# Kernel tuning notes

Measured on AMD Instinct MI355X. Metric: run time of the kernel, lower is better.

## Reference

```python
import jax, jax.numpy as jnp
import numpy as np

B, T, I, H = 128, 64, 128, 256
UNFOLDS = 6
EPS = 1e-08


def setup_inputs() -> dict:
    key = jax.random.key(0)
    ks = jax.random.split(key, 12)
    u = lambda k, sh, lo, hi: jax.random.uniform(k, sh, minval=lo, maxval=hi, dtype=jnp.float32)
    return {
        "x": jax.random.normal(ks[0], (B, T, I), dtype=jnp.float32),
        "input_weight": jnp.ones((I,), jnp.float32),
        "input_bias": jnp.zeros((I,), jnp.float32),
        "sensing_mu": u(ks[1], (I, H), 0.3, 0.8),
        "sensing_sigma": u(ks[2], (I, H), 3.0, 8.0),
        "sensing_w": u(ks[3], (I, H), 0.01, 1.0),
        "sensing_erev": 2.0 * jax.random.randint(ks[4], (I, H), 0, 2).astype(jnp.float32) - 1.0,
        "internal_mu": u(ks[5], (H, H), 0.3, 0.8),
        "internal_sigma": u(ks[6], (H, H), 3.0, 8.0),
        "internal_w": u(ks[7], (H, H), 0.01, 1.0),
        "internal_erev": 2.0 * jax.random.randint(ks[8], (H, H), 0, 2).astype(jnp.float32) - 1.0,
        "vleak": u(ks[9], (H,), -0.2, 0.2),
        "gleak": jnp.ones((H,), jnp.float32),
        "cm": jnp.ones((H,), jnp.float32) * 0.5,
        "output_weight": jnp.ones((H,), jnp.float32),
        "output_bias": jnp.zeros((H,), jnp.float32),
    }


def _gate(V, mu, sigma):
    # torch: sigmoid(sigma * (V.unsqueeze(-1) - mu)); V:[B,D] -> [B,D,H]
    return jax.nn.sigmoid(sigma * (V[..., None] - mu))


def reference(x, input_weight, input_bias, sensing_mu, sensing_sigma, sensing_w,
              sensing_erev, internal_mu, internal_sigma, internal_w, internal_erev,
              vleak, gleak, cm, output_weight, output_bias):
    # time_elapsed = 1.0 default -> cm_t = cm / (1/UNFOLDS) = cm * UNFOLDS
    cm_t = cm * UNFOLDS
    gl_vl = gleak * vleak

    def step(V, xt):
        # affine input mapping
        xm = xt * input_weight + input_bias                      # [B, I]
        s_act = sensing_w * _gate(xm, sensing_mu, sensing_sigma)  # [B, I, H]
        w_num_s = jnp.einsum('bih,ih->bh', s_act, sensing_erev)   # sum over I
        w_den_s = s_act.sum(axis=1)                               # [B, H]

        def unfold(Vc, _):
            w_act = internal_w * _gate(Vc, internal_mu, internal_sigma)  # [B, H, H]
            w_num = jnp.einsum('bij,ij->bj', w_act, internal_erev) + w_num_s
            w_den = w_act.sum(axis=1) + w_den_s
            Vn = (Vc * cm_t + gl_vl + w_num) / (cm_t + gleak + w_den + EPS)
            return Vn, None

        V, _ = jax.lax.scan(unfold, V, None, length=UNFOLDS)
        out_t = V * output_weight + output_bias
        return V, out_t

    h0 = jnp.zeros((x.shape[0], cm.shape[0]), x.dtype)
    hT, out = jax.lax.scan(step, h0, jnp.swapaxes(x, 0, 1))  # scan over T
    return jnp.swapaxes(out, 0, 1), hT  # ([B, T, H], [B, H])
```

## Files before the change

### kernel.cpp

```cpp
#include <hip/hip_runtime.h>
#include <hip/hip_fp16.h>

#define B_ 128
#define T_ 64
#define I_ 128
#define H_ 256
#define UF 6
#define EPSF 1e-8f

typedef _Float16 f16x2 __attribute__((ext_vector_type(2)));
union H2U { __half2 h; f16x2 v; unsigned u; };

static __device__ __forceinline__ float rcpf(float x) { return __builtin_amdgcn_rcpf(x); }
static __device__ __forceinline__ unsigned f2h(float f) { return (unsigned)__half_as_ushort(__float2half_rn(f)); }

#define GATE2(VW, AK, BK, WK, NM, DN) {                        \
    H2U v2_; v2_.u = (VW);                                     \
    H2U av_; av_.u = (AK);                                     \
    H2U bv_; bv_.u = (BK);                                     \
    __half2 z_ = __hfma2(av_.h, v2_.h, bv_.h);                 \
    __half2 e_ = h2exp2(z_);                                   \
    __half2 s_ = __hadd2(e_, __float2half2_rn(1.0f));          \
    H2U rv_; rv_.h = h2rcp(s_);                                \
    H2U ws_; ws_.u = (WK);                                     \
    H2U wa_; wa_.u = ws_.u & 0x7fff7fffu;                      \
    NM = __builtin_amdgcn_fdot2(ws_.v, rv_.v, NM, false);      \
    DN = __builtin_amdgcn_fdot2(wa_.v, rv_.v, DN, false);      \
}

__global__ __launch_bounds__(256) void pack_params(
    const float* __restrict__ smu, const float* __restrict__ ssig,
    const float* __restrict__ sw,  const float* __restrict__ serev,
    const float* __restrict__ imu, const float* __restrict__ isig,
    const float* __restrict__ iw,  const float* __restrict__ ierev,
    uint2* __restrict__ ABg, unsigned* __restrict__ Wg,
    uint2* __restrict__ SABg, unsigned* __restrict__ SWg,
    unsigned* __restrict__ Vg4)
{
    const float K = 1.4426950408889634f;
    int idx = blockIdx.x * 256 + threadIdx.x;
    {
        int jh = idx >> 14, rest = idx & 16383;
        int P = rest >> 7, jcol = rest & 127;
        int j = jcol ^ (((P >> 3) & 7) << 1);
        int jg = (jh << 7) + j;
        int i0 = 2 * P, i1 = i0 + 1;
        unsigned a0 = f2h(-isig[i0 * H_ + jg] * K);
        unsigned a1 = f2h(-isig[i1 * H_ + jg] * K);
        unsigned b0 = f2h(isig[i0 * H_ + jg] * imu[i0 * H_ + jg] * K);
        unsigned b1 = f2h(isig[i1 * H_ + jg] * imu[i1 * H_ + jg] * K);
        ABg[idx] = make_uint2(a0 | (a1 << 16), b0 | (b1 << 16));
    }
    {
        int P = idx >> 8, jg = idx & 255;
        int i0 = 2 * P, i1 = i0 + 1;
        unsigned w0 = f2h(iw[i0 * H_ + jg] * ierev[i0 * H_ + jg]);
        unsigned w1 = f2h(iw[i1 * H_ + jg] * ierev[i1 * H_ + jg]);
        Wg[idx] = w0 | (w1 << 16);
    }
    if (idx < 64 * H_) {
        int p = idx >> 8, jg = idx & 255;
        int i0 = 2 * p, i1 = i0 + 1;
        unsigned a0 = f2h(-ssig[i0 * H_ + jg] * K);
        unsigned a1 = f2h(-ssig[i1 * H_ + jg] * K);
        unsigned b0 = f2h(ssig[i0 * H_ + jg] * smu[i0 * H_ + jg] * K);
        unsigned b1 = f2h(ssig[i1 * H_ + jg] * smu[i1 * H_ + jg] * K);
        SABg[idx] = make_uint2(a0 | (a1 << 16), b0 | (b1 << 16));
        unsigned w0 = f2h(sw[i0 * H_ + jg] * serev[i0 * H_ + jg]);
        unsigned w1 = f2h(sw[i1 * H_ + jg] * serev[i1 * H_ + jg]);
        SWg[idx] = w0 | (w1 << 16);
    }
    Vg4[idx] = 0u;
    Vg4[idx + 32768] = 0u;
}

__global__ __launch_bounds__(1024)
__attribute__((amdgpu_waves_per_eu(4, 4)))
void ltc_rec(
    const float* __restrict__ x, const float* __restrict__ in_w, const float* __restrict__ in_b,
    const uint2* __restrict__ ABg, const unsigned* __restrict__ Wg,
    const uint2* __restrict__ SABg, const unsigned* __restrict__ SWg,
    const float* __restrict__ vleak, const float* __restrict__ gleak, const float* __restrict__ cm,
    const float* __restrict__ out_w, const float* __restrict__ out_b,
    unsigned* __restrict__ Vg4,
    float* __restrict__ out, float* __restrict__ hT)
{
    __shared__ __align__(16) unsigned char L[131840];
    unsigned* V2u = (unsigned*)(L + 131072);
    unsigned* xs2 = (unsigned*)(L + 131584);

    const int bx  = blockIdx.x;
    const int b   = bx & 127;
    const int jh  = bx >> 7;
    const int tid = threadIdx.x;
    const int c   = tid & 7;
    const int j   = tid >> 3;
    const int jg  = (jh << 7) + j;
    const int pjbase = (jh ^ 1) << 7;
    const int BH  = B_ * H_;

    {
        const uint4* src = (const uint4*)(ABg + ((size_t)jh << 14));
        uint4* dst = (uint4*)L;
        #pragma unroll
        for (int k = 0; k < 8; ++k) dst[tid + (k << 10)] = src[tid + (k << 10)];
    }

    unsigned rw[16];
    {
        const int po = (jh << 6) + (c << 3);
        const int pp = ((jh ^ 1) << 6) + (c << 3);
        #pragma unroll
        for (int k = 0; k < 8; ++k) {
            rw[k]     = Wg[((po + k) << 8) + jg];
            rw[8 + k] = Wg[((pp + k) << 8) + jg];
        }
    }

    const float cmt  = cm[jg] * (float)UF;
    const float gl   = gleak[jg];
    const float glvl = gl * vleak[jg];
    const float dc   = cmt + gl + EPSF;
    const float owj  = out_w[jg], obj = out_b[jg];
    float iw0 = 0.f, iw1 = 0.f, ib0 = 0.f, ib1 = 0.f;
    if (tid < 64) { iw0 = in_w[2 * tid]; iw1 = in_w[2 * tid + 1];
                    ib0 = in_b[2 * tid]; ib1 = in_b[2 * tid + 1]; }
    if (tid < 128) V2u[tid] = 0u;
    float vreg = 0.f;

    const float* xrow = x + (size_t)b * (T_ * I_);

    const int colb = (j ^ (c << 1)) << 3;
    const char* abA = (const char*)L + ((((jh << 6) + (c << 3))) << 10) + colb;
    const char* abB = (const char*)L + (((((jh ^ 1) << 6)) + (c << 3)) << 10) + colb;
    const int vbaseA = (jh << 6) + (c << 3);
    const int vbaseB = ((jh ^ 1) << 6) + (c << 3);
    const uint2* sabBase = SABg + ((c << 3) << 8) + jg;
    const unsigned* swBase = SWg + ((c << 3) << 8) + jg;

    for (int t = 0; t < T_; ++t) {
        if (tid < 64) {
            float2 xv = *(const float2*)(xrow + t * I_ + 2 * tid);
            H2U u_; u_.h = __floats2half2_rn(fmaf(xv.x, iw0, ib0), fmaf(xv.y, iw1, ib1));
            xs2[tid] = u_.u;
        }
        __syncthreads();

        float qsn = 0.f, qsd = 0.f;
        {
            const uint4 xa = *(const uint4*)(xs2 + (c << 3));
            const uint4 xb = *(const uint4*)(xs2 + (c << 3) + 4);
            #pragma unroll
            for (int k = 0; k < 8; ++k) {
                uint2 sab = sabBase[k << 8];
                unsigned swv = swBase[k << 8];
                unsigned xw = (k < 4) ? ((const unsigned*)&xa)[k] : ((const unsigned*)&xb)[k - 4];
                GATE2(xw, sab.x, sab.y, swv, qsn, qsd);
            }
        }

        for (int u = 0; u < UF; ++u) {
            const int p = t * UF + u + 1;
            float nm = qsn, dn = qsd;

            unsigned pv = 0; const unsigned* src = nullptr; unsigned want = 0;
            if (p > 1 && tid < 128) {
                want = (unsigned)(p - 1);
                src = Vg4 + (size_t)(want & 1) * BH + (b << 8) + pjbase + tid;
                pv = __hip_atomic_load(src, __ATOMIC_RELAXED, __HIP_MEMORY_SCOPE_AGENT);
            }

            {
                const uint4 va = *(const uint4*)(V2u + vbaseA);
                const uint4 vb = *(const uint4*)(V2u + vbaseA + 4);
                #pragma unroll
                for (int k = 0; k < 8; ++k) {
                    uint2 ab = *(const uint2*)(abA + (k << 10));
                    unsigned vw = (k < 4) ? ((const unsigned*)&va)[k] : ((const unsigned*)&vb)[k - 4];
                    GATE2(vw, ab.x, ab.y, rw[k], nm, dn);
                }
            }

            if (p > 1 && tid < 128) {
                while ((pv >> 16) != want)
                    pv = __hip_atomic_load(src, __ATOMIC_RELAXED, __HIP_MEMORY_SCOPE_AGENT);
                unsigned hv = pv & 0xffffu;
                unsigned hv1 = (unsigned)__shfl_down((int)hv, 1);
                if (!(tid & 1)) V2u[(pjbase >> 1) + (tid >> 1)] = hv | (hv1 << 16);
            }
            __syncthreads();

            {
                const uint4 va = *(const uint4*)(V2u + vbaseB);
                const uint4 vb = *(const uint4*)(V2u + vbaseB + 4);
                #pragma unroll
                for (int k = 0; k < 8; ++k) {
                    uint2 ab = *(const uint2*)(abB + (k << 10));
                    unsigned vw = (k < 4) ? ((const unsigned*)&va)[k] : ((const unsigned*)&vb)[k - 4];
                    GATE2(vw, ab.x, ab.y, rw[8 + k], nm, dn);
                }
            }

            nm += __shfl_xor(nm, 1); dn += __shfl_xor(dn, 1);
            nm += __shfl_xor(nm, 2); dn += __shfl_xor(dn, 2);
            nm += __shfl_xor(nm, 4); dn += __shfl_xor(dn, 4);

            float Vn = (fmaf(vreg, cmt, glvl) + nm) * rcpf(dn + dc);
            vreg = Vn;
            unsigned h0 = (unsigned)__half_as_ushort(__float2half_rn(Vn));
            if (c == 0)
                __hip_atomic_store(Vg4 + (size_t)(p & 1) * BH + (b << 8) + jg,
                                   ((unsigned)p << 16) | h0,
                                   __ATOMIC_RELAXED, __HIP_MEMORY_SCOPE_AGENT);
            unsigned h1 = (unsigned)__shfl_down((int)h0, 8);
            if (c == 0 && !(j & 1)) V2u[jg >> 1] = h0 | (h1 << 16);
            __syncthreads();
        }

        if (c == 0) out[((size_t)b * T_ + t) * H_ + jg] = fmaf(vreg, owj, obj);
    }
    if (c == 0) hT[(b << 8) + jg] = vreg;
}

extern "C" void kernel_launch(void* const* d_in, const int* in_sizes, int n_in,
                              void* d_out, int out_size, void* d_ws, size_t ws_size,
                              hipStream_t stream) {
    const float* x     = (const float*)d_in[0];
    const float* in_w  = (const float*)d_in[1];
    const float* in_b  = (const float*)d_in[2];
    const float* smu   = (const float*)d_in[3];
    const float* ssig  = (const float*)d_in[4];
    const float* sw    = (const float*)d_in[5];
    const float* serev = (const float*)d_in[6];
    const float* imu   = (const float*)d_in[7];
    const float* isig  = (const float*)d_in[8];
    const float* iw    = (const float*)d_in[9];
    const float* ierev = (const float*)d_in[10];
    const float* vleak = (const float*)d_in[11];
    const float* gleak = (const float*)d_in[12];
    const float* cmv   = (const float*)d_in[13];
    const float* ow    = (const float*)d_in[14];
    const float* ob    = (const float*)d_in[15];

    float* out = (float*)d_out;
    float* hT  = out + (size_t)B_ * T_ * H_;

    char* w = (char*)d_ws;
    uint2*    ABg  = (uint2*)(w);
    unsigned* Wg   = (unsigned*)(w + (256 << 10));
    uint2*    SABg = (uint2*)(w + (384 << 10));
    unsigned* SWg  = (unsigned*)(w + (512 << 10));
    unsigned* Vg4  = (unsigned*)(w + (576 << 10));

    pack_params<<<dim3(128), dim3(256), 0, stream>>>(
        smu, ssig, sw, serev, imu, isig, iw, ierev, ABg, Wg, SABg, SWg, Vg4);

    ltc_rec<<<dim3(256), dim3(1024), 0, stream>>>(
        x, in_w, in_b, ABg, Wg, SABg, SWg, vleak, gleak, cmv, ow, ob,
        Vg4, out, hT);
}
```

Measured before the change: 972.3 us.

## Pipeline next-step sensory gate into unfold loop and spread peer-V polling across waves

Computes the sensory gate contribution for timestep t+1 inside the six unfold iterations of step t. The eight input columns are split across the unfolds, and the x row is double-buffered in shared memory, which removes a barrier and a serial gate phase from each timestep. Polling for the partner block's V values now uses 8 lanes in each of the 16 waves with a wave-wide __all check, instead of 128 threads in the first two waves. Each thread writes its own 16-bit shared-memory entry, replacing the shuffle-and-pack step. The gain depends on hiding the extra global loads and gate work within the existing sync latency, at the cost of some added register pressure.

```diff
diff --git a/kernel.cpp b/kernel.cpp
--- a/kernel.cpp
+++ b/kernel.cpp
@@ -85,8 +85,8 @@
     unsigned* __restrict__ Vg4,
     float* __restrict__ out, float* __restrict__ hT)
 {
-    __shared__ __align__(16) unsigned char L[131840];
-    unsigned* V2u = (unsigned*)(L + 131072);
+    __shared__ __align__(16) unsigned char L[132096];
+    unsigned short* V2s = (unsigned short*)(L + 131072);
     unsigned* xs2 = (unsigned*)(L + 131584);
 
     const int bx  = blockIdx.x;
@@ -96,6 +96,8 @@
     const int c   = tid & 7;
     const int j   = tid >> 3;
     const int jg  = (jh << 7) + j;
+    const int wv  = tid >> 6;
+    const int Ln  = tid & 63;
     const int pjbase = (jh ^ 1) << 7;
     const int BH  = B_ * H_;
 
@@ -125,7 +127,7 @@
     float iw0 = 0.f, iw1 = 0.f, ib0 = 0.f, ib1 = 0.f;
     if (tid < 64) { iw0 = in_w[2 * tid]; iw1 = in_w[2 * tid + 1];
                     ib0 = in_b[2 * tid]; ib1 = in_b[2 * tid + 1]; }
-    if (tid < 128) V2u[tid] = 0u;
+    if (tid < 128) ((unsigned*)V2s)[tid] = 0u;
     float vreg = 0.f;
 
     const float* xrow = x + (size_t)b * (T_ * I_);
@@ -135,44 +137,63 @@
     const char* abB = (const char*)L + (((((jh ^ 1) << 6)) + (c << 3)) << 10) + colb;
     const int vbaseA = (jh << 6) + (c << 3);
     const int vbaseB = ((jh ^ 1) << 6) + (c << 3);
+    const unsigned* V2w = (const unsigned*)V2s;
     const uint2* sabBase = SABg + ((c << 3) << 8) + jg;
     const unsigned* swBase = SWg + ((c << 3) << 8) + jg;
 
+    if (tid < 64) {
+        float2 xv = *(const float2*)(xrow + 2 * tid);
+        H2U u_; u_.h = __floats2half2_rn(fmaf(xv.x, iw0, ib0), fmaf(xv.y, iw1, ib1));
+        xs2[tid] = u_.u;
+    }
+    __syncthreads();
+    float qsn = 0.f, qsd = 0.f;
+    {
+        const uint4 xa = *(const uint4*)(xs2 + (c << 3));
+        const uint4 xb = *(const uint4*)(xs2 + (c << 3) + 4);
+        #pragma unroll
+        for (int k = 0; k < 8; ++k) {
+            uint2 sab = sabBase[k << 8];
+            unsigned swv = swBase[k << 8];
+            unsigned xw = (k < 4) ? ((const unsigned*)&xa)[k] : ((const unsigned*)&xb)[k - 4];
+            GATE2(xw, sab.x, sab.y, swv, qsn, qsd);
+        }
+    }
+
     for (int t = 0; t < T_; ++t) {
-        if (tid < 64) {
-            float2 xv = *(const float2*)(xrow + t * I_ + 2 * tid);
+        const bool hasNext = (t + 1 < T_);
+        unsigned* xsNxt = xs2 + (((t + 1) & 1) << 6);
+        if (hasNext && tid < 64) {
+            float2 xv = *(const float2*)(xrow + (t + 1) * I_ + 2 * tid);
             H2U u_; u_.h = __floats2half2_rn(fmaf(xv.x, iw0, ib0), fmaf(xv.y, iw1, ib1));
-            xs2[tid] = u_.u;
-        }
-        __syncthreads();
-
-        float qsn = 0.f, qsd = 0.f;
-        {
-            const uint4 xa = *(const uint4*)(xs2 + (c << 3));
-            const uint4 xb = *(const uint4*)(xs2 + (c << 3) + 4);
-            #pragma unroll
-            for (int k = 0; k < 8; ++k) {
-                uint2 sab = sabBase[k << 8];
-                unsigned swv = swBase[k << 8];
-                unsigned xw = (k < 4) ? ((const unsigned*)&xa)[k] : ((const unsigned*)&xb)[k - 4];
-                GATE2(xw, sab.x, sab.y, swv, qsn, qsd);
-            }
-        }
-
+            xsNxt[tid] = u_.u;
+        }
+        float qn2 = 0.f, qd2 = 0.f;
+
+        #pragma unroll
         for (int u = 0; u < UF; ++u) {
             const int p = t * UF + u + 1;
             float nm = qsn, dn = qsd;
 
-            unsigned pv = 0; const unsigned* src = nullptr; unsigned want = 0;
-            if (p > 1 && tid < 128) {
+            unsigned pv = 0; unsigned want = 0;
+            const unsigned* srcp = nullptr;
+            const bool mine = (Ln < 8);
+            if (p > 1) {
                 want = (unsigned)(p - 1);
-                src = Vg4 + (size_t)(want & 1) * BH + (b << 8) + pjbase + tid;
-                pv = __hip_atomic_load(src, __ATOMIC_RELAXED, __HIP_MEMORY_SCOPE_AGENT);
+                srcp = Vg4 + (size_t)(want & 1) * BH + (b << 8) + pjbase + (wv << 3) + (Ln & 7);
+                if (mine) pv = __hip_atomic_load(srcp, __ATOMIC_RELAXED, __HIP_MEMORY_SCOPE_AGENT);
+            }
+
+            uint2 sp0 = make_uint2(0u, 0u), sp1 = make_uint2(0u, 0u);
+            unsigned sv0 = 0, sv1 = 0;
+            if (hasNext) {
+                sp0 = sabBase[u << 8]; sv0 = swBase[u << 8];
+                if (u >= 4) { sp1 = sabBase[(u + 2) << 8]; sv1 = swBase[(u + 2) << 8]; }
             }
 
             {
-                const uint4 va = *(const uint4*)(V2u + vbaseA);
-                const uint4 vb = *(const uint4*)(V2u + vbaseA + 4);
+                const uint4 va = *(const uint4*)(V2w + vbaseA);
+                const uint4 vb = *(const uint4*)(V2w + vbaseA + 4);
                 #pragma unroll
                 for (int k = 0; k < 8; ++k) {
                     uint2 ab = *(const uint2*)(abA + (k << 10));
@@ -181,18 +202,28 @@
                 }
             }
 
-            if (p > 1 && tid < 128) {
-                while ((pv >> 16) != want)
-                    pv = __hip_atomic_load(src, __ATOMIC_RELAXED, __HIP_MEMORY_SCOPE_AGENT);
-                unsigned hv = pv & 0xffffu;
-                unsigned hv1 = (unsigned)__shfl_down((int)hv, 1);
-                if (!(tid & 1)) V2u[(pjbase >> 1) + (tid >> 1)] = hv | (hv1 << 16);
+            if (p > 1) {
+                while (1) {
+                    bool ok = !mine || ((pv >> 16) == want);
+                    if (__all((int)ok)) break;
+                    if (mine) pv = __hip_atomic_load(srcp, __ATOMIC_RELAXED, __HIP_MEMORY_SCOPE_AGENT);
+                }
+                if (mine) V2s[pjbase + (wv << 3) + (Ln & 7)] = (unsigned short)(pv & 0xffffu);
             }
             __syncthreads();
 
+            if (hasNext) {
+                unsigned xw0 = xsNxt[(c << 3) + u];
+                GATE2(xw0, sp0.x, sp0.y, sv0, qn2, qd2);
+                if (u >= 4) {
+                    unsigned xw1 = xsNxt[(c << 3) + u + 2];
+                    GATE2(xw1, sp1.x, sp1.y, sv1, qn2, qd2);
+                }
+            }
+
             {
-                const uint4 va = *(const uint4*)(V2u + vbaseB);
-                const uint4 vb = *(const uint4*)(V2u + vbaseB + 4);
+                const uint4 va = *(const uint4*)(V2w + vbaseB);
+                const uint4 vb = *(const uint4*)(V2w + vbaseB + 4);
                 #pragma unroll
                 for (int k = 0; k < 8; ++k) {
                     uint2 ab = *(const uint2*)(abB + (k << 10));
@@ -208,15 +239,16 @@
             float Vn = (fmaf(vreg, cmt, glvl) + nm) * rcpf(dn + dc);
             vreg = Vn;
             unsigned h0 = (unsigned)__half_as_ushort(__float2half_rn(Vn));
-            if (c == 0)
+            if (c == 0) {
                 __hip_atomic_store(Vg4 + (size_t)(p & 1) * BH + (b << 8) + jg,
                                    ((unsigned)p << 16) | h0,
                                    __ATOMIC_RELAXED, __HIP_MEMORY_SCOPE_AGENT);
-            unsigned h1 = (unsigned)__shfl_down((int)h0, 8);
-            if (c == 0 && !(j & 1)) V2u[jg >> 1] = h0 | (h1 << 16);
+                V2s[jg] = (unsigned short)h0;
+            }
             __syncthreads();
         }
 
+        if (hasNext) { qsn = qn2; qsd = qd2; }
         if (c == 0) out[((size_t)b * T_ + t) * H_ + jg] = fmaf(vreg, owj, obj);
     }
     if (c == 0) hT[(b << 8) + jg] = vreg;
```

Measured after the change: 1.390 ms. 43.0% more time.

## Split hidden units across four cooperating blocks per batch row instead of two

Applied to the files above, without the earlier changes.

Each batch row's 256 hidden units are now split into four 64-column quarters, each handled by its own block (512 blocks total). Each thread now covers 16 input rows, so per-thread register weights and LDS parameter storage are halved. The gate tiles are re-swizzled and reordered so the block's own quarter is processed first while the other three quarters' states are fetched through flag-tagged global exchanges. More blocks in flight should raise per-step parallelism and occupancy, at the cost of more cross-block synchronization traffic and a spin-wait on three peer blocks instead of one.

```diff
diff --git a/kernel.cpp b/kernel.cpp
--- a/kernel.cpp
+++ b/kernel.cpp
@@ -33,23 +33,24 @@
     const float* __restrict__ sw,  const float* __restrict__ serev,
     const float* __restrict__ imu, const float* __restrict__ isig,
     const float* __restrict__ iw,  const float* __restrict__ ierev,
-    uint2* __restrict__ ABg, unsigned* __restrict__ Wg,
+    uint2* __restrict__ ABq, unsigned* __restrict__ Wg,
     uint2* __restrict__ SABg, unsigned* __restrict__ SWg,
     unsigned* __restrict__ Vg4)
 {
     const float K = 1.4426950408889634f;
     int idx = blockIdx.x * 256 + threadIdx.x;
     {
-        int jh = idx >> 14, rest = idx & 16383;
-        int P = rest >> 7, jcol = rest & 127;
-        int j = jcol ^ (((P >> 3) & 7) << 1);
-        int jg = (jh << 7) + j;
-        int i0 = 2 * P, i1 = i0 + 1;
+        int q = idx >> 13, pp = (idx >> 6) & 127, jcol = idx & 63;
+        int k = pp >> 4, c = pp & 15;
+        int ip = (((q + (k >> 1)) & 3) << 5) + ((k & 1) << 4) + c;
+        int j = jcol ^ ((pp & 7) << 3);
+        int jg = (q << 6) + j;
+        int i0 = 2 * ip, i1 = i0 + 1;
         unsigned a0 = f2h(-isig[i0 * H_ + jg] * K);
         unsigned a1 = f2h(-isig[i1 * H_ + jg] * K);
         unsigned b0 = f2h(isig[i0 * H_ + jg] * imu[i0 * H_ + jg] * K);
         unsigned b1 = f2h(isig[i1 * H_ + jg] * imu[i1 * H_ + jg] * K);
-        ABg[idx] = make_uint2(a0 | (a1 << 16), b0 | (b1 << 16));
+        ABq[idx] = make_uint2(a0 | (a1 << 16), b0 | (b1 << 16));
     }
     {
         int P = idx >> 8, jg = idx & 255;
@@ -75,46 +76,43 @@
 }
 
 __global__ __launch_bounds__(1024)
-__attribute__((amdgpu_waves_per_eu(4, 4)))
+__attribute__((amdgpu_waves_per_eu(8, 8)))
 void ltc_rec(
     const float* __restrict__ x, const float* __restrict__ in_w, const float* __restrict__ in_b,
-    const uint2* __restrict__ ABg, const unsigned* __restrict__ Wg,
+    const uint2* __restrict__ ABq, const unsigned* __restrict__ Wg,
     const uint2* __restrict__ SABg, const unsigned* __restrict__ SWg,
     const float* __restrict__ vleak, const float* __restrict__ gleak, const float* __restrict__ cm,
     const float* __restrict__ out_w, const float* __restrict__ out_b,
     unsigned* __restrict__ Vg4,
     float* __restrict__ out, float* __restrict__ hT)
 {
-    __shared__ __align__(16) unsigned char L[131840];
-    unsigned* V2u = (unsigned*)(L + 131072);
-    unsigned* xs2 = (unsigned*)(L + 131584);
+    __shared__ __align__(16) unsigned char L[66304];
+    unsigned* V2u = (unsigned*)(L + 65536);
+    unsigned* xs2 = (unsigned*)(L + 66048);
 
     const int bx  = blockIdx.x;
     const int b   = bx & 127;
-    const int jh  = bx >> 7;
+    const int q   = bx >> 7;
     const int tid = threadIdx.x;
-    const int c   = tid & 7;
-    const int j   = tid >> 3;
-    const int jg  = (jh << 7) + j;
-    const int pjbase = (jh ^ 1) << 7;
+    const int c   = tid & 15;
+    const int j   = tid >> 4;
+    const int jg  = (q << 6) + j;
+    const int wv  = tid >> 6;
+    const int Ln  = tid & 63;
     const int BH  = B_ * H_;
 
     {
-        const uint4* src = (const uint4*)(ABg + ((size_t)jh << 14));
+        const uint4* src = (const uint4*)(ABq + ((size_t)q << 13));
         uint4* dst = (uint4*)L;
         #pragma unroll
-        for (int k = 0; k < 8; ++k) dst[tid + (k << 10)] = src[tid + (k << 10)];
-    }
-
-    unsigned rw[16];
-    {
-        const int po = (jh << 6) + (c << 3);
-        const int pp = ((jh ^ 1) << 6) + (c << 3);
-        #pragma unroll
-        for (int k = 0; k < 8; ++k) {
-            rw[k]     = Wg[((po + k) << 8) + jg];
-            rw[8 + k] = Wg[((pp + k) << 8) + jg];
-        }
+        for (int k = 0; k < 4; ++k) dst[tid + (k << 10)] = src[tid + (k << 10)];
+    }
+
+    unsigned rw[8];
+    #pragma unroll
+    for (int k = 0; k < 8; ++k) {
+        int ip = (((q + (k >> 1)) & 3) << 5) + ((k & 1) << 4) + c;
+        rw[k] = Wg[(ip << 8) + jg];
     }
 
     const float cmt  = cm[jg] * (float)UF;
@@ -130,13 +128,12 @@
 
     const float* xrow = x + (size_t)b * (T_ * I_);
 
-    const int colb = (j ^ (c << 1)) << 3;
-    const char* abA = (const char*)L + ((((jh << 6) + (c << 3))) << 10) + colb;
-    const char* abB = (const char*)L + (((((jh ^ 1) << 6)) + (c << 3)) << 10) + colb;
-    const int vbaseA = (jh << 6) + (c << 3);
-    const int vbaseB = ((jh ^ 1) << 6) + (c << 3);
-    const uint2* sabBase = SABg + ((c << 3) << 8) + jg;
-    const unsigned* swBase = SWg + ((c << 3) << 8) + jg;
+    const char* abBase = (const char*)L + (c << 9) + ((j ^ ((c & 7) << 3)) << 3);
+    int vq[4];
+    #pragma unroll
+    for (int d = 0; d < 4; ++d) vq[d] = (((q + d) & 3) << 5) + c;
+    const uint2* sabBase = SABg + ((c << 2) << 8) + jg;
+    const unsigned* swBase = SWg + ((c << 2) << 8) + jg;
 
     for (int t = 0; t < T_; ++t) {
         if (tid < 64) {
@@ -147,63 +144,54 @@
         __syncthreads();
 
         float qsn = 0.f, qsd = 0.f;
-        {
-            const uint4 xa = *(const uint4*)(xs2 + (c << 3));
-            const uint4 xb = *(const uint4*)(xs2 + (c << 3) + 4);
-            #pragma unroll
-            for (int k = 0; k < 8; ++k) {
-                uint2 sab = sabBase[k << 8];
-                unsigned swv = swBase[k << 8];
-                unsigned xw = (k < 4) ? ((const unsigned*)&xa)[k] : ((const unsigned*)&xb)[k - 4];
-                GATE2(xw, sab.x, sab.y, swv, qsn, qsd);
-            }
+        #pragma unroll
+        for (int m = 0; m < 4; ++m) {
+            uint2 sab = sabBase[m << 8];
+            unsigned swv = swBase[m << 8];
+            unsigned xw = xs2[(c << 2) + m];
+            GATE2(xw, sab.x, sab.y, swv, qsn, qsd);
         }
 
         for (int u = 0; u < UF; ++u) {
             const int p = t * UF + u + 1;
             float nm = qsn, dn = qsd;
 
-            unsigned pv = 0; const unsigned* src = nullptr; unsigned want = 0;
-            if (p > 1 && tid < 128) {
+            unsigned pv = 0, want = 0; const unsigned* srcp = nullptr; int pjg = 0;
+            const bool mine = (wv < 3);
+            if (p > 1 && mine) {
                 want = (unsigned)(p - 1);
-                src = Vg4 + (size_t)(want & 1) * BH + (b << 8) + pjbase + tid;
-                pv = __hip_atomic_load(src, __ATOMIC_RELAXED, __HIP_MEMORY_SCOPE_AGENT);
-            }
-
-            {
-                const uint4 va = *(const uint4*)(V2u + vbaseA);
-                const uint4 vb = *(const uint4*)(V2u + vbaseA + 4);
-                #pragma unroll
-                for (int k = 0; k < 8; ++k) {
-                    uint2 ab = *(const uint2*)(abA + (k << 10));
-                    unsigned vw = (k < 4) ? ((const unsigned*)&va)[k] : ((const unsigned*)&vb)[k - 4];
-                    GATE2(vw, ab.x, ab.y, rw[k], nm, dn);
-                }
-            }
-
-            if (p > 1 && tid < 128) {
+                pjg = (((q + 1 + wv) & 3) << 6) + Ln;
+                srcp = Vg4 + (size_t)(want & 1) * BH + (b << 8) + pjg;
+                pv = __hip_atomic_load(srcp, __ATOMIC_RELAXED, __HIP_MEMORY_SCOPE_AGENT);
+            }
+
+            #pragma unroll
+            for (int k = 0; k < 2; ++k) {
+                unsigned vw = V2u[vq[0] + ((k & 1) << 4)];
+                uint2 ab = *(const uint2*)(abBase + (k << 13));
+                GATE2(vw, ab.x, ab.y, rw[k], nm, dn);
+            }
+
+            if (p > 1 && mine) {
                 while ((pv >> 16) != want)
-                    pv = __hip_atomic_load(src, __ATOMIC_RELAXED, __HIP_MEMORY_SCOPE_AGENT);
+                    pv = __hip_atomic_load(srcp, __ATOMIC_RELAXED, __HIP_MEMORY_SCOPE_AGENT);
                 unsigned hv = pv & 0xffffu;
                 unsigned hv1 = (unsigned)__shfl_down((int)hv, 1);
-                if (!(tid & 1)) V2u[(pjbase >> 1) + (tid >> 1)] = hv | (hv1 << 16);
+                if (!(Ln & 1)) V2u[pjg >> 1] = hv | (hv1 << 16);
             }
             __syncthreads();
 
-            {
-                const uint4 va = *(const uint4*)(V2u + vbaseB);
-                const uint4 vb = *(const uint4*)(V2u + vbaseB + 4);
-                #pragma unroll
-                for (int k = 0; k < 8; ++k) {
-                    uint2 ab = *(const uint2*)(abB + (k << 10));
-                    unsigned vw = (k < 4) ? ((const unsigned*)&va)[k] : ((const unsigned*)&vb)[k - 4];
-                    GATE2(vw, ab.x, ab.y, rw[8 + k], nm, dn);
-                }
+            #pragma unroll
+            for (int k = 2; k < 8; ++k) {
+                unsigned vw = V2u[vq[k >> 1] + ((k & 1) << 4)];
+                uint2 ab = *(const uint2*)(abBase + (k << 13));
+                GATE2(vw, ab.x, ab.y, rw[k], nm, dn);
             }
 
             nm += __shfl_xor(nm, 1); dn += __shfl_xor(dn, 1);
             nm += __shfl_xor(nm, 2); dn += __shfl_xor(dn, 2);
             nm += __shfl_xor(nm, 4); dn += __shfl_xor(dn, 4);
+            nm += __shfl_xor(nm, 8); dn += __shfl_xor(dn, 8);
 
             float Vn = (fmaf(vreg, cmt, glvl) + nm) * rcpf(dn + dc);
             vreg = Vn;
@@ -212,7 +200,7 @@
                 __hip_atomic_store(Vg4 + (size_t)(p & 1) * BH + (b << 8) + jg,
                                    ((unsigned)p << 16) | h0,
                                    __ATOMIC_RELAXED, __HIP_MEMORY_SCOPE_AGENT);
-            unsigned h1 = (unsigned)__shfl_down((int)h0, 8);
+            unsigned h1 = (unsigned)__shfl_down((int)h0, 16);
             if (c == 0 && !(j & 1)) V2u[jg >> 1] = h0 | (h1 << 16);
             __syncthreads();
         }
@@ -246,16 +234,16 @@
     float* hT  = out + (size_t)B_ * T_ * H_;
 
     char* w = (char*)d_ws;
-    uint2*    ABg  = (uint2*)(w);
+    uint2*    ABq  = (uint2*)(w);
     unsigned* Wg   = (unsigned*)(w + (256 << 10));
     uint2*    SABg = (uint2*)(w + (384 << 10));
     unsigned* SWg  = (unsigned*)(w + (512 << 10));
     unsigned* Vg4  = (unsigned*)(w + (576 << 10));
 
     pack_params<<<dim3(128), dim3(256), 0, stream>>>(
-        smu, ssig, sw, serev, imu, isig, iw, ierev, ABg, Wg, SABg, SWg, Vg4);
-
-    ltc_rec<<<dim3(256), dim3(1024), 0, stream>>>(
-        x, in_w, in_b, ABg, Wg, SABg, SWg, vleak, gleak, cmv, ow, ob,
+        smu, ssig, sw, serev, imu, isig, iw, ierev, ABq, Wg, SABg, SWg, Vg4);
+
+    ltc_rec<<<dim3(512), dim3(1024), 0, stream>>>(
+        x, in_w, in_b, ABq, Wg, SABg, SWg, vleak, gleak, cmv, ow, ob,
         Vg4, out, hT);
 }
```

After: 2.015 ms. 2.07x slower.
